# Kernel optimization log

Measured on AMD Instinct MI355X. Metric: run time of the kernel, lower is better.

Reference implementation:

```python
import jax, jax.numpy as jnp
import numpy as np

B, T, M, D, H, DK, DV = 2, 1024, 1024, 1024, 16, 64, 64
R = 2 * T + M  # number of relative positions required by rel_shift path


def setup_inputs() -> dict:
    key = jax.random.key(0)
    ks = jax.random.split(key, 11)
    s = 0.02
    return {
        "inputs": jax.random.normal(ks[0], (B, T, D), jnp.float32),
        "attention_mask": jnp.ones((B, T, M + T), jnp.float32),
        "positional_encodings": jax.random.normal(ks[1], (R, D), jnp.float32),
        "memory": jax.random.normal(ks[2], (B, M, D), jnp.float32),
        "Wq": jax.random.normal(ks[3], (D, H * DK), jnp.float32) * s,
        "Wk": jax.random.normal(ks[4], (D, H * DK), jnp.float32) * s,
        "Wv": jax.random.normal(ks[5], (D, H * DV), jnp.float32) * s,
        "Wr": jax.random.normal(ks[6], (D, H * DK), jnp.float32) * s,
        "r_w_bias": jax.random.normal(ks[7], (H, DK), jnp.float32) * s,
        "r_r_bias": jax.random.normal(ks[8], (H, DK), jnp.float32) * s,
        "W_out": jax.random.normal(ks[9], (H * DV, D), jnp.float32) * s,
    }


def _rel_shift(m, attention_length):
    # m: [T_q, T_q + L] -> [T_q, L], TXL relative shift via reshape/slice
    tq, total = m.shape
    x = m.reshape(total, tq)[1:].reshape(tq, total - 1)
    return x[:, :attention_length]


def reference(inputs, attention_mask, positional_encodings, memory,
              Wq, Wk, Wv, Wr, r_w_bias, r_r_bias, W_out):
    b, t, d = inputs.shape
    values = jnp.concatenate([memory, inputs], axis=1)  # [B, L, D]
    L = values.shape[1]
    q = (inputs @ Wq).reshape(b, t, H, DK)
    k = (values @ Wk).reshape(b, L, H, DK)
    v = (values @ Wv).reshape(b, L, H, DV)
    rk = (positional_encodings @ Wr).reshape(-1, H, DK)  # [R, H, DK]
    # content + relative logits (TXL)
    content = jnp.einsum('bthd,bThd->bhtT', q + r_w_bias, k)        # [B,H,T,L]
    rel = jnp.einsum('bthd,rhd->bhtr', q + r_r_bias, rk)            # [B,H,T,R]
    rel = jax.vmap(jax.vmap(lambda m: _rel_shift(m, L)))(rel)       # [B,H,T,L]
    logits = (content + rel) * (DK ** -0.5)
    masked = logits - (1.0 - attention_mask[:, None, :, :]) * 1e30
    w = jax.nn.softmax(masked, axis=-1)
    attn = jnp.einsum('bhtT,bThd->bthd', w, v)                      # [B,T,H,DV]
    return attn.reshape(b, t, H * DV) @ W_out
```

## Files before the change

### kernel.cpp

```cpp
#include <hip/hip_runtime.h>
#include <hip/hip_fp16.h>
#include <stdint.h>

#define Bz 2
#define Tq 1024
#define Mm 1024
#define Hh 16
#define Ll 2048
#define Rr 3072

typedef __attribute__((ext_vector_type(8))) short bf16x8;
typedef __attribute__((ext_vector_type(4))) float f32x4;

typedef __attribute__((address_space(3))) uint8_t lds_u8_t;
typedef __attribute__((address_space(1))) uint8_t glb_u8_t;

__device__ __forceinline__ void gl2lds16(const void* g, void* l) {
  __builtin_amdgcn_global_load_lds((const glb_u8_t*)g, (lds_u8_t*)l, 16, 0, 0);
}

__device__ __forceinline__ unsigned short f2bf(float f) {
  unsigned int u = __builtin_bit_cast(unsigned int, f);
  u = u + 0x7fffu + ((u >> 16) & 1u);
  return (unsigned short)(u >> 16);
}
__device__ __forceinline__ float b2f(unsigned short s) {
  unsigned int u = ((unsigned int)s) << 16;
  return __builtin_bit_cast(float, u);
}

__global__ __launch_bounds__(256) void k_prep(const float* __restrict__ x,
                                              const float* __restrict__ mem,
                                              const float* __restrict__ pos,
                                              const float* __restrict__ mask,
                                              unsigned short* __restrict__ vin,
                                              unsigned short* __restrict__ pb,
                                              unsigned short* __restrict__ mb) {
  int bid = blockIdx.x;
  if (bid < 4096) {
    int idx = bid * 256 + threadIdx.x;
    int e = idx << 2;
    int row = e >> 10, col = e & 1023;
    int b = row >> 11, l = row & 2047;
    const float* s = (l < Mm) ? (mem + (((size_t)b * Mm + l) << 10) + col)
                              : (x + (((size_t)b * Tq + (l - Mm)) << 10) + col);
    float4 v = *(const float4*)s;
    ushort4 o;
    o.x = f2bf(v.x); o.y = f2bf(v.y); o.z = f2bf(v.z); o.w = f2bf(v.w);
    *(ushort4*)(vin + e) = o;
  } else if (bid < 7168) {
    int idx = (bid - 4096) * 256 + threadIdx.x;
    int e = idx << 2;
    float4 v = *(const float4*)(pos + e);
    ushort4 t;
    t.x = f2bf(v.x); t.y = f2bf(v.y); t.z = f2bf(v.z); t.w = f2bf(v.w);
    *(ushort4*)(pb + e) = t;
  } else {
    int idx = (bid - 7168) * 256 + threadIdx.x;
    int e = idx << 2;
    const float BIGM = 1.442695e30f;
    float4 v = *(const float4*)(mask + e);
    ushort4 t;
    t.x = f2bf((1.0f - v.x) * BIGM); t.y = f2bf((1.0f - v.y) * BIGM);
    t.z = f2bf((1.0f - v.z) * BIGM); t.w = f2bf((1.0f - v.w) * BIGM);
    *(ushort4*)(mb + e) = t;
  }
}

__global__ __launch_bounds__(256) void k_wtall(
    const float* __restrict__ w0, const float* __restrict__ w1,
    const float* __restrict__ w2, const float* __restrict__ w3,
    const float* __restrict__ w4,
    unsigned short* __restrict__ t0, unsigned short* __restrict__ t1,
    unsigned short* __restrict__ t2, unsigned short* __restrict__ t3,
    unsigned short* __restrict__ t4) {
  const float* W;
  unsigned short* WT;
  switch (blockIdx.z) {
    case 0: W = w0; WT = t0; break;
    case 1: W = w1; WT = t1; break;
    case 2: W = w2; WT = t2; break;
    case 3: W = w3; WT = t3; break;
    default: W = w4; WT = t4; break;
  }
  __shared__ float tile[64][65];
  int k0 = blockIdx.x * 64, n0 = blockIdx.y * 64;
  int tid = threadIdx.x;
  int rr = tid >> 4, c4 = (tid & 15) * 4;
#pragma unroll
  for (int it = 0; it < 4; ++it) {
    int r = rr + it * 16;
    float4 v = *(const float4*)(W + (size_t)(k0 + r) * 1024 + n0 + c4);
    tile[r][c4] = v.x; tile[r][c4 + 1] = v.y;
    tile[r][c4 + 2] = v.z; tile[r][c4 + 3] = v.w;
  }
  __syncthreads();
#pragma unroll
  for (int it = 0; it < 4; ++it) {
    int n = rr + it * 16;
    ushort4 o;
    o.x = f2bf(tile[c4 + 0][n]); o.y = f2bf(tile[c4 + 1][n]);
    o.z = f2bf(tile[c4 + 2][n]); o.w = f2bf(tile[c4 + 3][n]);
    *(ushort4*)(WT + (size_t)(n0 + n) * 1024 + k0 + c4) = o;
  }
}

template <int RMAP>
__device__ __forceinline__ void gemm_core(const unsigned short* __restrict__ A,
                                          const unsigned short* __restrict__ Bt,
                                          int m0, int n0, unsigned short* As,
                                          unsigned short* Bs, f32x4 acc[4][4]) {
  const int tid = threadIdx.x;
  const int w = tid >> 6, lane = tid & 63;
  const int quad = lane >> 4, li = lane & 15;
  const int wr = w >> 1, wc = w & 1;
  f32x4 z = {0.f, 0.f, 0.f, 0.f};
#pragma unroll
  for (int mi = 0; mi < 4; ++mi)
#pragma unroll
    for (int ni = 0; ni < 4; ++ni) acc[mi][ni] = z;

  const int rs = lane >> 2;
  const int cs = lane & 3;

  for (int k0 = 0; k0 < 1024; k0 += 32) {
    __syncthreads();
#pragma unroll
    for (int s = 0; s < 2; ++s) {
      int i = w * 2 + s;
      int r = i * 16 + rs;
      int c = cs ^ ((r >> 1) & 3);
      int ar = m0 + r;
      if (RMAP) ar = ar + 1024 + (ar & 1024);
      gl2lds16(A + (size_t)ar * 1024 + k0 + c * 8, (char*)As + i * 1024);
      int br = n0 + r;
      gl2lds16(Bt + (size_t)br * 1024 + k0 + c * 8, (char*)Bs + i * 1024);
    }
    __syncthreads();
    bf16x8 af[4], bfr[4];
#pragma unroll
    for (int mi = 0; mi < 4; ++mi) {
      int r = wr * 64 + mi * 16 + li;
      int ch = quad ^ ((r >> 1) & 3);
      af[mi] = *(const bf16x8*)((const char*)As + r * 64 + ch * 16);
    }
#pragma unroll
    for (int ni = 0; ni < 4; ++ni) {
      int r = wc * 64 + ni * 16 + li;
      int ch = quad ^ ((r >> 1) & 3);
      bfr[ni] = *(const bf16x8*)((const char*)Bs + r * 64 + ch * 16);
    }
#pragma unroll
    for (int mi = 0; mi < 4; ++mi)
#pragma unroll
      for (int ni = 0; ni < 4; ++ni)
        acc[mi][ni] = __builtin_amdgcn_mfma_f32_16x16x32_bf16(
            af[mi], bfr[ni], acc[mi][ni], 0, 0, 0);
  }
}

__global__ __launch_bounds__(256) void k_proj(
    const unsigned short* __restrict__ Vin, const unsigned short* __restrict__ Pb,
    const unsigned short* __restrict__ WqT, const unsigned short* __restrict__ WkT,
    const unsigned short* __restrict__ WvT, const unsigned short* __restrict__ WrT,
    const float* __restrict__ rwb, const float* __restrict__ rrb,
    unsigned short* __restrict__ qwb, unsigned short* __restrict__ qrb,
    unsigned short* __restrict__ kb, unsigned short* __restrict__ vtb,
    unsigned short* __restrict__ rkb) {
  __shared__ unsigned short As[128 * 32];
  __shared__ unsigned short Bs[128 * 32];
  const int t = blockIdx.x;
  const int tid = threadIdx.x, w = tid >> 6, lane = tid & 63;
  const int quad = lane >> 4, li = lane & 15, wr = w >> 1, wc = w & 1;
  f32x4 acc[4][4];

  if (t < 256) {
    int m0 = (t >> 3) * 128, n0 = (t & 7) * 128;
    gemm_core<0>(Vin, WkT, m0, n0, As, Bs, acc);
#pragma unroll
    for (int mi = 0; mi < 4; ++mi)
#pragma unroll
      for (int ni = 0; ni < 4; ++ni)
#pragma unroll
        for (int reg = 0; reg < 4; ++reg) {
          int rrow = m0 + wr * 64 + mi * 16 + quad * 4 + reg;
          int cc = n0 + wc * 64 + ni * 16 + li;
          kb[(size_t)rrow * 1024 + cc] = f2bf(acc[mi][ni][reg]);
        }
  } else if (t < 512) {
    int tt = t - 256;
    int m0 = (tt >> 3) * 128, n0 = (tt & 7) * 128;
    gemm_core<0>(Vin, WvT, m0, n0, As, Bs, acc);
#pragma unroll
    for (int mi = 0; mi < 4; ++mi)
#pragma unroll
      for (int ni = 0; ni < 4; ++ni) {
        int r0 = m0 + wr * 64 + mi * 16 + quad * 4;
        int b = r0 >> 11, l0 = r0 & 2047;
        int cc = n0 + wc * 64 + ni * 16 + li;
        ushort4 o;
        o.x = f2bf(acc[mi][ni][0]); o.y = f2bf(acc[mi][ni][1]);
        o.z = f2bf(acc[mi][ni][2]); o.w = f2bf(acc[mi][ni][3]);
        *(ushort4*)(vtb + ((size_t)(b * 1024 + cc)) * Ll + l0) = o;
      }
  } else if (t < 640) {
    int tt = t - 512;
    int m0 = (tt >> 3) * 128, n0 = (tt & 7) * 128;
    gemm_core<1>(Vin, WqT, m0, n0, As, Bs, acc);
#pragma unroll
    for (int mi = 0; mi < 4; ++mi)
#pragma unroll
      for (int ni = 0; ni < 4; ++ni) {
        int cc = n0 + wc * 64 + ni * 16 + li;
        float bw_ = rwb[cc], br_ = rrb[cc];
#pragma unroll
        for (int reg = 0; reg < 4; ++reg) {
          int rrow = m0 + wr * 64 + mi * 16 + quad * 4 + reg;
          size_t off = (size_t)rrow * 1024 + cc;
          qwb[off] = f2bf(acc[mi][ni][reg] + bw_);
          qrb[off] = f2bf(acc[mi][ni][reg] + br_);
        }
      }
  } else {
    int tt = t - 640;
    int m0 = (tt >> 3) * 128, n0 = (tt & 7) * 128;
    gemm_core<0>(Pb, WrT, m0, n0, As, Bs, acc);
#pragma unroll
    for (int mi = 0; mi < 4; ++mi)
#pragma unroll
      for (int ni = 0; ni < 4; ++ni)
#pragma unroll
        for (int reg = 0; reg < 4; ++reg) {
          int rrow = m0 + wr * 64 + mi * 16 + quad * 4 + reg;
          int cc = n0 + wc * 64 + ni * 16 + li;
          rkb[(size_t)rrow * 1024 + cc] = f2bf(acc[mi][ni][reg]);
        }
  }
}

__global__ __launch_bounds__(256) void k_gemm_out64(
    const unsigned short* __restrict__ attnb, const unsigned short* __restrict__ WoT,
    float* __restrict__ out) {
  __shared__ unsigned short As[64 * 32];
  __shared__ unsigned short Bs[128 * 32];
  int m0 = blockIdx.x * 64, n0 = blockIdx.y * 128;
  const int tid = threadIdx.x, w = tid >> 6, lane = tid & 63;
  const int quad = lane >> 4, li = lane & 15, wr = w >> 1, wc = w & 1;
  f32x4 z = {0.f, 0.f, 0.f, 0.f};
  f32x4 acc[2][4];
#pragma unroll
  for (int mi = 0; mi < 2; ++mi)
#pragma unroll
    for (int ni = 0; ni < 4; ++ni) acc[mi][ni] = z;
  const int rs = lane >> 2, cs = lane & 3;
  for (int k0 = 0; k0 < 1024; k0 += 32) {
    __syncthreads();
    {
      int r = w * 16 + rs;
      int c = cs ^ ((r >> 1) & 3);
      gl2lds16(attnb + (size_t)(m0 + r) * 1024 + k0 + c * 8, (char*)As + w * 1024);
    }
#pragma unroll
    for (int s = 0; s < 2; ++s) {
      int i = w * 2 + s;
      int r = i * 16 + rs;
      int c = cs ^ ((r >> 1) & 3);
      gl2lds16(WoT + (size_t)(n0 + r) * 1024 + k0 + c * 8, (char*)Bs + i * 1024);
    }
    __syncthreads();
    bf16x8 af[2], bfr[4];
#pragma unroll
    for (int mi = 0; mi < 2; ++mi) {
      int r = wr * 32 + mi * 16 + li;
      int ch = quad ^ ((r >> 1) & 3);
      af[mi] = *(const bf16x8*)((const char*)As + r * 64 + ch * 16);
    }
#pragma unroll
    for (int ni = 0; ni < 4; ++ni) {
      int r = wc * 64 + ni * 16 + li;
      int ch = quad ^ ((r >> 1) & 3);
      bfr[ni] = *(const bf16x8*)((const char*)Bs + r * 64 + ch * 16);
    }
#pragma unroll
    for (int mi = 0; mi < 2; ++mi)
#pragma unroll
      for (int ni = 0; ni < 4; ++ni)
        acc[mi][ni] = __builtin_amdgcn_mfma_f32_16x16x32_bf16(
            af[mi], bfr[ni], acc[mi][ni], 0, 0, 0);
  }
#pragma unroll
  for (int mi = 0; mi < 2; ++mi)
#pragma unroll
    for (int ni = 0; ni < 4; ++ni)
#pragma unroll
      for (int reg = 0; reg < 4; ++reg) {
        int rrow = m0 + wr * 32 + mi * 16 + quad * 4 + reg;
        int cc = n0 + wc * 64 + ni * 16 + li;
        out[(size_t)rrow * 1024 + cc] = acc[mi][ni][reg];
      }
}

__global__ __launch_bounds__(256, 2) void k_attn(
    const unsigned short* __restrict__ qw, const unsigned short* __restrict__ qr,
    const unsigned short* __restrict__ kb, const unsigned short* __restrict__ vt,
    const unsigned short* __restrict__ rkb, const unsigned short* __restrict__ mb,
    unsigned short* __restrict__ attnb) {
  __shared__ unsigned short Ks[2][64 * 64];
  __shared__ unsigned short Vs[2][64 * 64];
  __shared__ unsigned short Rs[256 * 64];
  __shared__ unsigned short Sb[4][16 * 72];

  const int tid = threadIdx.x;
  const int w = tid >> 6, lane = tid & 63;
  const int quad = lane >> 4, li = lane & 15;
  const int qt = blockIdx.x, h = blockIdx.y, b = blockIdx.z;
  const int t0blk = qt * 64;
  const int t0w = t0blk + w * 16;
  const int rboff = 48 - 16 * w;
  const int rbase0 = Tq - t0blk - 63;

  bf16x8 aqw[2], aqr[2];
  {
    const unsigned short* p1 = qw + ((size_t)((b * Tq + t0w + li) * Hh + h)) * 64;
    aqw[0] = *(const bf16x8*)(p1 + quad * 8);
    aqw[1] = *(const bf16x8*)(p1 + 32 + quad * 8);
    const unsigned short* p2 = qr + ((size_t)((b * Tq + t0w + li) * Hh + h)) * 64;
    aqr[0] = *(const bf16x8*)(p2 + quad * 8);
    aqr[1] = *(const bf16x8*)(p2 + 32 + quad * 8);
  }

  f32x4 z = {0.f, 0.f, 0.f, 0.f};
  f32x4 o[4];
  o[0] = z; o[1] = z; o[2] = z; o[3] = z;
  f32x4 ol = z;

  const int srow = lane >> 3;
  const int scs = lane & 7;
  const float SC = 0.125f * 1.4426950408889634f;
  const short oneb = 0x3F80;
  const bf16x8 onesf = {oneb, oneb, oneb, oneb, oneb, oneb, oneb, oneb};

  unsigned short* pw = &Sb[w][0];
  const unsigned short* mrowA = mb + ((size_t)(b * Tq + t0w + li)) * Ll;
  int srcl[4];
#pragma unroll
  for (int reg = 0; reg < 4; ++reg) {
    int row = quad * 4 + reg;
    srcl[reg] = (lane & 48) + ((li + row + 1) & 15);
  }

#pragma unroll
  for (int s = 0; s < 4; ++s) {
    int i = w * 4 + s;
    int r = i * 8 + srow;
    int gr = rbase0 + r;
    if (gr > Rr - 1) gr = Rr - 1;
    int c = scs ^ (r & 7);
    gl2lds16(rkb + ((size_t)gr * Hh + h) * 64 + c * 8, (char*)Rs + i * 1024);
  }
#pragma unroll
  for (int s = 0; s < 2; ++s) {
    int i = w * 2 + s;
    int r = i * 8 + srow;
    int c = scs ^ (r & 7);
    gl2lds16(kb + ((size_t)((b * Ll + r) * Hh + h)) * 64 + c * 8,
             (char*)Ks[0] + i * 1024);
    gl2lds16(vt + ((size_t)((b * Hh + h) * 64 + r)) * Ll + c * 8,
             (char*)Vs[0] + i * 1024);
  }

  for (int jt = 0; jt < 32; ++jt) {
    const int j0 = jt * 64;
    const int cur = jt & 1, nxt = cur ^ 1;
    __builtin_amdgcn_s_waitcnt(0x0F70);
    __syncthreads();
    bf16x8 mv0 = *(const bf16x8*)(mrowA + j0 + quad * 8);
    bf16x8 mv1 = *(const bf16x8*)(mrowA + j0 + 32 + quad * 8);
    asm volatile("" ::: "memory");
    if (jt < 31) {
      const int j0n = j0 + 64;
#pragma unroll
      for (int s = 0; s < 2; ++s) {
        int i = w * 2 + s;
        int r = i * 8 + srow;
        int c = scs ^ (r & 7);
        gl2lds16(kb + ((size_t)((b * Ll + j0n + r) * Hh + h)) * 64 + c * 8,
                 (char*)Ks[nxt] + i * 1024);
        gl2lds16(vt + ((size_t)((b * Hh + h) * 64 + r)) * Ll + j0n + c * 8,
                 (char*)Vs[nxt] + i * 1024);
      }
#pragma unroll
      for (int s = 0; s < 2; ++s) {
        int i2 = w * 2 + s;
        int rr = i2 * 8 + srow;
        int ofs = j0 + 128 + rr;
        int gr = rbase0 + ofs;
        if (gr > Rr - 1) gr = Rr - 1;
        int ring = ofs & 255;
        int c = scs ^ (rr & 7);
        gl2lds16(rkb + ((size_t)gr * Hh + h) * 64 + c * 8, (char*)Rs + ring * 128);
      }
    }
    const unsigned short* KsC = Ks[cur];
    const unsigned short* VsC = Vs[cur];
    f32x4 sc[4];
    sc[0] = z; sc[1] = z; sc[2] = z; sc[3] = z;
#pragma unroll
    for (int ks = 0; ks < 2; ++ks)
#pragma unroll
      for (int nt = 0; nt < 4; ++nt) {
        int j = nt * 16 + li;
        int ch = (ks * 4 + quad) ^ (j & 7);
        bf16x8 kf = *(const bf16x8*)((const char*)KsC + j * 128 + ch * 16);
        sc[nt] = __builtin_amdgcn_mfma_f32_16x16x32_bf16(aqw[ks], kf, sc[nt], 0, 0, 0);
      }
    f32x4 bd[5];
    bd[0] = z; bd[1] = z; bd[2] = z; bd[3] = z; bd[4] = z;
#pragma unroll
    for (int ks = 0; ks < 2; ++ks)
#pragma unroll
      for (int nt = 0; nt < 5; ++nt) {
        int pr = (rboff + nt * 16 + li + j0) & 255;
        int ch = (ks * 4 + quad) ^ (pr & 7);
        bf16x8 rf = *(const bf16x8*)((const char*)Rs + pr * 128 + ch * 16);
        bd[nt] = __builtin_amdgcn_mfma_f32_16x16x32_bf16(aqr[ks], rf, bd[nt], 0, 0, 0);
      }
    float rot[4][4];
#pragma unroll
    for (int nt = 0; nt < 4; ++nt)
#pragma unroll
      for (int reg = 0; reg < 4; ++reg)
        rot[nt][reg] = __shfl(sc[nt][reg], srcl[reg], 64);
#pragma unroll
    for (int nt = 0; nt < 5; ++nt)
#pragma unroll
      for (int reg = 0; reg < 4; ++reg) {
        int row = quad * 4 + reg;
        int jj = nt * 16 + li + row - 15;
        int ntlo = (nt == 0) ? 3 : (nt - 1);
        int nthi = (nt > 3) ? 0 : nt;
        float val = ((li + row) >= 15) ? rot[nthi][reg] : rot[ntlo][reg];
        float s = val + bd[nt][reg];
        if ((unsigned)jj < 64u)
          pw[row * 72 + jj] = __builtin_bit_cast(unsigned short, __float2half(s));
      }
    __builtin_amdgcn_s_waitcnt(0xc07f);
#pragma unroll
    for (int ks = 0; ks < 2; ++ks) {
      const int cofs = ks * 32 + quad * 8;
      ushort4 s0 = *(const ushort4*)(pw + li * 72 + cofs);
      ushort4 s1 = *(const ushort4*)(pw + li * 72 + cofs + 4);
      bf16x8 mv = ks ? mv1 : mv0;
      unsigned short su[8] = {s0.x, s0.y, s0.z, s0.w, s1.x, s1.y, s1.z, s1.w};
      bf16x8 ap;
#pragma unroll
      for (int i2 = 0; i2 < 8; ++i2) {
        float sf = __half2float(__builtin_bit_cast(__half, su[i2]));
        float mvf = b2f((unsigned short)mv[i2]);
        float p = exp2f(sf * SC - mvf);
        ap[i2] = (short)f2bf(p);
      }
      ol = __builtin_amdgcn_mfma_f32_16x16x32_bf16(ap, onesf, ol, 0, 0, 0);
#pragma unroll
      for (int nt = 0; nt < 4; ++nt) {
        int dv = nt * 16 + li;
        int ch = (ks * 4 + quad) ^ (dv & 7);
        bf16x8 vf = *(const bf16x8*)((const char*)VsC + dv * 128 + ch * 16);
        o[nt] = __builtin_amdgcn_mfma_f32_16x16x32_bf16(ap, vf, o[nt], 0, 0, 0);
      }
    }
  }
  float inv[4];
#pragma unroll
  for (int reg = 0; reg < 4; ++reg) inv[reg] = 1.0f / ol[reg];
#pragma unroll
  for (int nt = 0; nt < 4; ++nt)
#pragma unroll
    for (int reg = 0; reg < 4; ++reg) {
      int trow = t0w + quad * 4 + reg;
      attnb[((size_t)(b * Tq + trow)) * 1024 + h * 64 + nt * 16 + li] =
          f2bf(o[nt][reg] * inv[reg]);
    }
}

extern "C" void kernel_launch(void* const* d_in, const int* in_sizes, int n_in,
                              void* d_out, int out_size, void* d_ws, size_t ws_size,
                              hipStream_t stream) {
  const float* x = (const float*)d_in[0];
  const float* mask = (const float*)d_in[1];
  const float* pos = (const float*)d_in[2];
  const float* mem = (const float*)d_in[3];
  const float* Wq = (const float*)d_in[4];
  const float* Wk = (const float*)d_in[5];
  const float* Wv = (const float*)d_in[6];
  const float* Wr = (const float*)d_in[7];
  const float* rwb = (const float*)d_in[8];
  const float* rrb = (const float*)d_in[9];
  const float* Wo = (const float*)d_in[10];
  float* out = (float*)d_out;

  uint8_t* ws = (uint8_t*)d_ws;
  const size_t MB = 1024 * 1024;
  unsigned short* Vinb = (unsigned short*)(ws + 0);
  unsigned short* WqT = (unsigned short*)(ws + 8 * MB);
  unsigned short* WkT = (unsigned short*)(ws + 10 * MB);
  unsigned short* WvT = (unsigned short*)(ws + 12 * MB);
  unsigned short* WrT = (unsigned short*)(ws + 14 * MB);
  unsigned short* WoT = (unsigned short*)(ws + 16 * MB);
  unsigned short* Pb = (unsigned short*)(ws + 18 * MB);
  unsigned short* qwb = (unsigned short*)(ws + 24 * MB);
  unsigned short* qrb = (unsigned short*)(ws + 28 * MB);
  unsigned short* kb = (unsigned short*)(ws + 32 * MB);
  unsigned short* vtb = (unsigned short*)(ws + 40 * MB);
  unsigned short* rkb = (unsigned short*)(ws + 48 * MB);
  unsigned short* mbb = (unsigned short*)(ws + 54 * MB);
  unsigned short* attnb = (unsigned short*)(ws + 19 * MB);

  hipLaunchKernelGGL(k_prep, dim3(11264), dim3(256), 0, stream,
                     x, mem, pos, mask, Vinb, Pb, mbb);
  hipLaunchKernelGGL(k_wtall, dim3(16, 16, 5), dim3(256), 0, stream,
                     Wq, Wk, Wv, Wr, Wo, WqT, WkT, WvT, WrT, WoT);
  hipLaunchKernelGGL(k_proj, dim3(832), dim3(256), 0, stream,
                     Vinb, Pb, WqT, WkT, WvT, WrT, rwb, rrb, qwb, qrb, kb, vtb, rkb);
  hipLaunchKernelGGL(k_attn, dim3(16, 16, 2), dim3(256), 0, stream,
                     qwb, qrb, kb, vtb, rkb, mbb, attnb);
  hipLaunchKernelGGL(k_gemm_out64, dim3(32, 8), dim3(256), 0, stream,
                     attnb, WoT, out);
}
```

Baseline: 265.6 us.

## Fuse prep kernels, share A tile across K/V projections, apply Q biases in attention

After: 269.3 us. Within noise of the previous version (+1.4%).

```diff
diff --git a/kernel.cpp b/kernel.cpp
--- a/kernel.cpp
+++ b/kernel.cpp
@@ -29,13 +29,18 @@
   return __builtin_bit_cast(float, u);
 }
 
-__global__ __launch_bounds__(256) void k_prep(const float* __restrict__ x,
-                                              const float* __restrict__ mem,
-                                              const float* __restrict__ pos,
-                                              const float* __restrict__ mask,
-                                              unsigned short* __restrict__ vin,
-                                              unsigned short* __restrict__ pb,
-                                              unsigned short* __restrict__ mb) {
+__global__ __launch_bounds__(256) void k_prep2(
+    const float* __restrict__ x, const float* __restrict__ mem,
+    const float* __restrict__ pos, const float* __restrict__ mask,
+    const float* __restrict__ w0, const float* __restrict__ w1,
+    const float* __restrict__ w2, const float* __restrict__ w3,
+    const float* __restrict__ w4,
+    unsigned short* __restrict__ vin, unsigned short* __restrict__ pb,
+    unsigned short* __restrict__ mb,
+    unsigned short* __restrict__ t0, unsigned short* __restrict__ t1,
+    unsigned short* __restrict__ t2, unsigned short* __restrict__ t3,
+    unsigned short* __restrict__ t4) {
+  __shared__ float tile[64][65];
   int bid = blockIdx.x;
   if (bid < 4096) {
     int idx = bid * 256 + threadIdx.x;
@@ -55,7 +60,7 @@
     ushort4 t;
     t.x = f2bf(v.x); t.y = f2bf(v.y); t.z = f2bf(v.z); t.w = f2bf(v.w);
     *(ushort4*)(pb + e) = t;
-  } else {
+  } else if (bid < 11264) {
     int idx = (bid - 7168) * 256 + threadIdx.x;
     int e = idx << 2;
     const float BIGM = 1.442695e30f;
@@ -64,44 +69,37 @@
     t.x = f2bf((1.0f - v.x) * BIGM); t.y = f2bf((1.0f - v.y) * BIGM);
     t.z = f2bf((1.0f - v.z) * BIGM); t.w = f2bf((1.0f - v.w) * BIGM);
     *(ushort4*)(mb + e) = t;
-  }
-}
-
-__global__ __launch_bounds__(256) void k_wtall(
-    const float* __restrict__ w0, const float* __restrict__ w1,
-    const float* __restrict__ w2, const float* __restrict__ w3,
-    const float* __restrict__ w4,
-    unsigned short* __restrict__ t0, unsigned short* __restrict__ t1,
-    unsigned short* __restrict__ t2, unsigned short* __restrict__ t3,
-    unsigned short* __restrict__ t4) {
-  const float* W;
-  unsigned short* WT;
-  switch (blockIdx.z) {
-    case 0: W = w0; WT = t0; break;
-    case 1: W = w1; WT = t1; break;
-    case 2: W = w2; WT = t2; break;
-    case 3: W = w3; WT = t3; break;
-    default: W = w4; WT = t4; break;
-  }
-  __shared__ float tile[64][65];
-  int k0 = blockIdx.x * 64, n0 = blockIdx.y * 64;
-  int tid = threadIdx.x;
-  int rr = tid >> 4, c4 = (tid & 15) * 4;
-#pragma unroll
-  for (int it = 0; it < 4; ++it) {
-    int r = rr + it * 16;
-    float4 v = *(const float4*)(W + (size_t)(k0 + r) * 1024 + n0 + c4);
-    tile[r][c4] = v.x; tile[r][c4 + 1] = v.y;
-    tile[r][c4 + 2] = v.z; tile[r][c4 + 3] = v.w;
-  }
-  __syncthreads();
-#pragma unroll
-  for (int it = 0; it < 4; ++it) {
-    int n = rr + it * 16;
-    ushort4 o;
-    o.x = f2bf(tile[c4 + 0][n]); o.y = f2bf(tile[c4 + 1][n]);
-    o.z = f2bf(tile[c4 + 2][n]); o.w = f2bf(tile[c4 + 3][n]);
-    *(ushort4*)(WT + (size_t)(n0 + n) * 1024 + k0 + c4) = o;
+  } else {
+    int r3 = bid - 11264;
+    int mz = r3 >> 8, rem = r3 & 255;
+    const float* W;
+    unsigned short* WT;
+    switch (mz) {
+      case 0: W = w0; WT = t0; break;
+      case 1: W = w1; WT = t1; break;
+      case 2: W = w2; WT = t2; break;
+      case 3: W = w3; WT = t3; break;
+      default: W = w4; WT = t4; break;
+    }
+    int k0 = (rem >> 4) * 64, n0 = (rem & 15) * 64;
+    int tid = threadIdx.x;
+    int rr = tid >> 4, c4 = (tid & 15) * 4;
+#pragma unroll
+    for (int it = 0; it < 4; ++it) {
+      int r = rr + it * 16;
+      float4 v = *(const float4*)(W + (size_t)(k0 + r) * 1024 + n0 + c4);
+      tile[r][c4] = v.x; tile[r][c4 + 1] = v.y;
+      tile[r][c4 + 2] = v.z; tile[r][c4 + 3] = v.w;
+    }
+    __syncthreads();
+#pragma unroll
+    for (int it = 0; it < 4; ++it) {
+      int n = rr + it * 16;
+      ushort4 o;
+      o.x = f2bf(tile[c4 + 0][n]); o.y = f2bf(tile[c4 + 1][n]);
+      o.z = f2bf(tile[c4 + 2][n]); o.w = f2bf(tile[c4 + 3][n]);
+      *(ushort4*)(WT + (size_t)(n0 + n) * 1024 + k0 + c4) = o;
+    }
   }
 }
 
@@ -159,24 +157,86 @@
   }
 }
 
-__global__ __launch_bounds__(256) void k_proj(
+__global__ __launch_bounds__(256, 2) void k_proj(
     const unsigned short* __restrict__ Vin, const unsigned short* __restrict__ Pb,
     const unsigned short* __restrict__ WqT, const unsigned short* __restrict__ WkT,
     const unsigned short* __restrict__ WvT, const unsigned short* __restrict__ WrT,
-    const float* __restrict__ rwb, const float* __restrict__ rrb,
-    unsigned short* __restrict__ qwb, unsigned short* __restrict__ qrb,
-    unsigned short* __restrict__ kb, unsigned short* __restrict__ vtb,
-    unsigned short* __restrict__ rkb) {
+    unsigned short* __restrict__ qb, unsigned short* __restrict__ kb,
+    unsigned short* __restrict__ vtb, unsigned short* __restrict__ rkb) {
   __shared__ unsigned short As[128 * 32];
   __shared__ unsigned short Bs[128 * 32];
+  __shared__ unsigned short Bs2[128 * 32];
   const int t = blockIdx.x;
   const int tid = threadIdx.x, w = tid >> 6, lane = tid & 63;
   const int quad = lane >> 4, li = lane & 15, wr = w >> 1, wc = w & 1;
-  f32x4 acc[4][4];
+  f32x4 z = {0.f, 0.f, 0.f, 0.f};
 
   if (t < 256) {
     int m0 = (t >> 3) * 128, n0 = (t & 7) * 128;
-    gemm_core<0>(Vin, WkT, m0, n0, As, Bs, acc);
+    f32x4 ak[4][4], av[4][4];
+#pragma unroll
+    for (int mi = 0; mi < 4; ++mi)
+#pragma unroll
+      for (int ni = 0; ni < 4; ++ni) { ak[mi][ni] = z; av[mi][ni] = z; }
+    const int rs = lane >> 2, cs = lane & 3;
+    for (int k0 = 0; k0 < 1024; k0 += 32) {
+      __syncthreads();
+#pragma unroll
+      for (int s = 0; s < 2; ++s) {
+        int i = w * 2 + s;
+        int r = i * 16 + rs;
+        int c = cs ^ ((r >> 1) & 3);
+        gl2lds16(Vin + (size_t)(m0 + r) * 1024 + k0 + c * 8, (char*)As + i * 1024);
+        gl2lds16(WkT + (size_t)(n0 + r) * 1024 + k0 + c * 8, (char*)Bs + i * 1024);
+        gl2lds16(WvT + (size_t)(n0 + r) * 1024 + k0 + c * 8, (char*)Bs2 + i * 1024);
+      }
+      __syncthreads();
+      bf16x8 af[4], bk[4], bv[4];
+#pragma unroll
+      for (int mi = 0; mi < 4; ++mi) {
+        int r = wr * 64 + mi * 16 + li;
+        int ch = quad ^ ((r >> 1) & 3);
+        af[mi] = *(const bf16x8*)((const char*)As + r * 64 + ch * 16);
+      }
+#pragma unroll
+      for (int ni = 0; ni < 4; ++ni) {
+        int r = wc * 64 + ni * 16 + li;
+        int ch = quad ^ ((r >> 1) & 3);
+        bk[ni] = *(const bf16x8*)((const char*)Bs + r * 64 + ch * 16);
+        bv[ni] = *(const bf16x8*)((const char*)Bs2 + r * 64 + ch * 16);
+      }
+#pragma unroll
+      for (int mi = 0; mi < 4; ++mi)
+#pragma unroll
+        for (int ni = 0; ni < 4; ++ni) {
+          ak[mi][ni] = __builtin_amdgcn_mfma_f32_16x16x32_bf16(
+              af[mi], bk[ni], ak[mi][ni], 0, 0, 0);
+          av[mi][ni] = __builtin_amdgcn_mfma_f32_16x16x32_bf16(
+              af[mi], bv[ni], av[mi][ni], 0, 0, 0);
+        }
+    }
+#pragma unroll
+    for (int mi = 0; mi < 4; ++mi)
+#pragma unroll
+      for (int ni = 0; ni < 4; ++ni) {
+        int cc = n0 + wc * 64 + ni * 16 + li;
+#pragma unroll
+        for (int reg = 0; reg < 4; ++reg) {
+          int rrow = m0 + wr * 64 + mi * 16 + quad * 4 + reg;
+          kb[(size_t)rrow * 1024 + cc] = f2bf(ak[mi][ni][reg]);
+        }
+        int r0 = m0 + wr * 64 + mi * 16 + quad * 4;
+        int b = r0 >> 11, l0 = r0 & 2047;
+        ushort4 o;
+        o.x = f2bf(av[mi][ni][0]); o.y = f2bf(av[mi][ni][1]);
+        o.z = f2bf(av[mi][ni][2]); o.w = f2bf(av[mi][ni][3]);
+        *(ushort4*)(vtb + ((size_t)(b * 1024 + cc)) * Ll + l0) = o;
+      }
+  } else if (t < 384) {
+    int tt = t - 256;
+    int m0 = (tt >> 3) * 128, n0 = (tt & 7) * 128;
+    f32x4 acc[4][4];
+    gemm_core<1>(Vin, WqT, m0, n0, As, Bs, acc);
 #pragma unroll
     for (int mi = 0; mi < 4; ++mi)
 #pragma unroll
@@ -185,45 +245,12 @@
         for (int reg = 0; reg < 4; ++reg) {
           int rrow = m0 + wr * 64 + mi * 16 + quad * 4 + reg;
           int cc = n0 + wc * 64 + ni * 16 + li;
-          kb[(size_t)rrow * 1024 + cc] = f2bf(acc[mi][ni][reg]);
+          qb[(size_t)rrow * 1024 + cc] = f2bf(acc[mi][ni][reg]);
         }
-  } else if (t < 512) {
-    int tt = t - 256;
+  } else {
+    int tt = t - 384;
     int m0 = (tt >> 3) * 128, n0 = (tt & 7) * 128;
-    gemm_core<0>(Vin, WvT, m0, n0, As, Bs, acc);
-#pragma unroll
-    for (int mi = 0; mi < 4; ++mi)
-#pragma unroll
-      for (int ni = 0; ni < 4; ++ni) {
-        int r0 = m0 + wr * 64 + mi * 16 + quad * 4;
-        int b = r0 >> 11, l0 = r0 & 2047;
-        int cc = n0 + wc * 64 + ni * 16 + li;
-        ushort4 o;
-        o.x = f2bf(acc[mi][ni][0]); o.y = f2bf(acc[mi][ni][1]);
-        o.z = f2bf(acc[mi][ni][2]); o.w = f2bf(acc[mi][ni][3]);
-        *(ushort4*)(vtb + ((size_t)(b * 1024 + cc)) * Ll + l0) = o;
-      }
-  } else if (t < 640) {
-    int tt = t - 512;
-    int m0 = (tt >> 3) * 128, n0 = (tt & 7) * 128;
-    gemm_core<1>(Vin, WqT, m0, n0, As, Bs, acc);
-#pragma unroll
-    for (int mi = 0; mi < 4; ++mi)
-#pragma unroll
-      for (int ni = 0; ni < 4; ++ni) {
-        int cc = n0 + wc * 64 + ni * 16 + li;
-        float bw_ = rwb[cc], br_ = rrb[cc];
-#pragma unroll
-        for (int reg = 0; reg < 4; ++reg) {
-          int rrow = m0 + wr * 64 + mi * 16 + quad * 4 + reg;
-          size_t off = (size_t)rrow * 1024 + cc;
-          qwb[off] = f2bf(acc[mi][ni][reg] + bw_);
-          qrb[off] = f2bf(acc[mi][ni][reg] + br_);
-        }
-      }
-  } else {
-    int tt = t - 640;
-    int m0 = (tt >> 3) * 128, n0 = (tt & 7) * 128;
+    f32x4 acc[4][4];
     gemm_core<0>(Pb, WrT, m0, n0, As, Bs, acc);
 #pragma unroll
     for (int mi = 0; mi < 4; ++mi)
@@ -301,7 +328,8 @@
 }
 
 __global__ __launch_bounds__(256, 2) void k_attn(
-    const unsigned short* __restrict__ qw, const unsigned short* __restrict__ qr,
+    const unsigned short* __restrict__ qb, const float* __restrict__ rwb,
+    const float* __restrict__ rrb,
     const unsigned short* __restrict__ kb, const unsigned short* __restrict__ vt,
     const unsigned short* __restrict__ rkb, const unsigned short* __restrict__ mb,
     unsigned short* __restrict__ attnb) {
@@ -321,12 +349,23 @@
 
   bf16x8 aqw[2], aqr[2];
   {
-    const unsigned short* p1 = qw + ((size_t)((b * Tq + t0w + li) * Hh + h)) * 64;
-    aqw[0] = *(const bf16x8*)(p1 + quad * 8);
-    aqw[1] = *(const bf16x8*)(p1 + 32 + quad * 8);
-    const unsigned short* p2 = qr + ((size_t)((b * Tq + t0w + li) * Hh + h)) * 64;
-    aqr[0] = *(const bf16x8*)(p2 + quad * 8);
-    aqr[1] = *(const bf16x8*)(p2 + 32 + quad * 8);
+    const unsigned short* p1 = qb + ((size_t)((b * Tq + t0w + li) * Hh + h)) * 64;
+#pragma unroll
+    for (int ks = 0; ks < 2; ++ks) {
+      bf16x8 qf = *(const bf16x8*)(p1 + ks * 32 + quad * 8);
+      const float* wp = rwb + h * 64 + ks * 32 + quad * 8;
+      const float* rp = rrb + h * 64 + ks * 32 + quad * 8;
+      float4 w0 = *(const float4*)wp, w1 = *(const float4*)(wp + 4);
+      float4 r0 = *(const float4*)rp, r1 = *(const float4*)(rp + 4);
+      float wv[8] = {w0.x, w0.y, w0.z, w0.w, w1.x, w1.y, w1.z, w1.w};
+      float rv[8] = {r0.x, r0.y, r0.z, r0.w, r1.x, r1.y, r1.z, r1.w};
+#pragma unroll
+      for (int i2 = 0; i2 < 8; ++i2) {
+        float qv = b2f((unsigned short)qf[i2]);
+        aqw[ks][i2] = (short)f2bf(qv + wv[i2]);
+        aqr[ks][i2] = (short)f2bf(qv + rv[i2]);
+      }
+    }
   }
 
   f32x4 z = {0.f, 0.f, 0.f, 0.f};
@@ -508,22 +547,20 @@
   unsigned short* WrT = (unsigned short*)(ws + 14 * MB);
   unsigned short* WoT = (unsigned short*)(ws + 16 * MB);
   unsigned short* Pb = (unsigned short*)(ws + 18 * MB);
-  unsigned short* qwb = (unsigned short*)(ws + 24 * MB);
-  unsigned short* qrb = (unsigned short*)(ws + 28 * MB);
+  unsigned short* qb = (unsigned short*)(ws + 24 * MB);
   unsigned short* kb = (unsigned short*)(ws + 32 * MB);
   unsigned short* vtb = (unsigned short*)(ws + 40 * MB);
   unsigned short* rkb = (unsigned short*)(ws + 48 * MB);
   unsigned short* mbb = (unsigned short*)(ws + 54 * MB);
   unsigned short* attnb = (unsigned short*)(ws + 19 * MB);
 
-  hipLaunchKernelGGL(k_prep, dim3(11264), dim3(256), 0, stream,
-                     x, mem, pos, mask, Vinb, Pb, mbb);
-  hipLaunchKernelGGL(k_wtall, dim3(16, 16, 5), dim3(256), 0, stream,
-                     Wq, Wk, Wv, Wr, Wo, WqT, WkT, WvT, WrT, WoT);
-  hipLaunchKernelGGL(k_proj, dim3(832), dim3(256), 0, stream,
-                     Vinb, Pb, WqT, WkT, WvT, WrT, rwb, rrb, qwb, qrb, kb, vtb, rkb);
+  hipLaunchKernelGGL(k_prep2, dim3(12544), dim3(256), 0, stream,
+                     x, mem, pos, mask, Wq, Wk, Wv, Wr, Wo,
+                     Vinb, Pb, mbb, WqT, WkT, WvT, WrT, WoT);
+  hipLaunchKernelGGL(k_proj, dim3(576), dim3(256), 0, stream,
+                     Vinb, Pb, WqT, WkT, WvT, WrT, qb, kb, vtb, rkb);
   hipLaunchKernelGGL(k_attn, dim3(16, 16, 2), dim3(256), 0, stream,
-                     qwb, qrb, kb, vtb, rkb, mbb, attnb);
+                     qb, rwb, rrb, kb, vtb, rkb, mbb, attnb);
   hipLaunchKernelGGL(k_gemm_out64, dim3(32, 8), dim3(256), 0, stream,
                      attnb, WoT, out);
 }
```
